# Optimization experiments

Hardware: AMD Instinct MI355X
Metric: run time of the kernel (lower is better)

Reference implementation:

```python
import jax, jax.numpy as jnp
import numpy as np
from jax import lax

B, N, C = 16, 16384, 90      # batch, anchors, classes
K = 100                      # per-class pre-NMS top-k
MAX_DET = 100                # final detections per image
IOU_THR = 0.5
SCORE_THR = 0.05


def setup_inputs() -> dict:
    key = jax.random.key(0)
    k1, k2, k3, k4 = jax.random.split(key, 4)
    box_encodings = jax.random.normal(k1, (B, N, 4), dtype=jnp.float32) * 0.5
    class_logits = jax.random.normal(k2, (B, N, C), dtype=jnp.float32) * 2.0 - 3.0
    # anchors as [ymin,xmin,ymax,xmax] in normalized coords
    centers = jax.random.uniform(k3, (N, 2), dtype=jnp.float32)             # (cy,cx)
    sizes = jax.random.uniform(k4, (N, 2), dtype=jnp.float32, minval=0.05, maxval=0.3)
    anchors = jnp.concatenate([centers - sizes / 2, centers + sizes / 2], axis=-1)
    return {"box_encodings": box_encodings, "class_logits": class_logits, "anchors": anchors}


def decode_boxes(enc, anchors):
    ymin, xmin, ymax, xmax = [anchors[:, i] for i in range(4)]
    ha, wa = ymax - ymin, xmax - xmin
    cya, cxa = (ymin + ymax) / 2, (xmin + xmax) / 2
    ty, tx, th, tw = enc[..., 0] / 10.0, enc[..., 1] / 10.0, enc[..., 2] / 5.0, enc[..., 3] / 5.0
    cy = ty * ha + cya
    cx = tx * wa + cxa
    h = jnp.exp(th) * ha
    w = jnp.exp(tw) * wa
    boxes = jnp.stack([cy - h / 2, cx - w / 2, cy + h / 2, cx + w / 2], axis=-1)
    return jnp.clip(boxes, 0.0, 1.0)  # [..., N, 4]


def pairwise_iou(b):  # b: [K,4]
    area = jnp.maximum(b[:, 2] - b[:, 0], 0) * jnp.maximum(b[:, 3] - b[:, 1], 0)
    iy = jnp.maximum(jnp.minimum(b[:, None, 2], b[None, :, 2]) - jnp.maximum(b[:, None, 0], b[None, :, 0]), 0)
    ix = jnp.maximum(jnp.minimum(b[:, None, 3], b[None, :, 3]) - jnp.maximum(b[:, None, 1], b[None, :, 1]), 0)
    inter = iy * ix
    union = area[:, None] + area[None, :] - inter
    return inter / jnp.maximum(union, 1e-8)


def nms_one_class(boxes, scores_c):  # boxes [N,4], scores_c [N]
    vals, idx = lax.top_k(scores_c, K)           # sorted descending
    bk = boxes[idx]                               # [K,4]
    iou = pairwise_iou(bk)                        # [K,K]
    def step(keep, i):
        supp = jnp.any(keep & (iou[i] >= IOU_THR))
        ki = (vals[i] > SCORE_THR) & (~supp)
        return keep.at[i].set(ki), None
    keep, _ = lax.scan(step, jnp.zeros((K,), bool), jnp.arange(K))
    return bk, vals * keep                        # suppressed -> score 0


def postprocess_one(boxes, scores):  # boxes [N,4], scores [N,C]
    bx_ck, sc_ck = jax.vmap(nms_one_class, in_axes=(None, 1))(boxes, scores)  # [C,K,4],[C,K]
    cls_ck = jnp.broadcast_to(jnp.arange(C, dtype=jnp.float32)[:, None], (C, K))
    sc_f = sc_ck.reshape(-1)
    fsc, fidx = lax.top_k(sc_f, MAX_DET)
    fbx = bx_ck.reshape(-1, 4)[fidx]
    fcl = cls_ck.reshape(-1)[fidx]
    return jnp.concatenate([fbx, fcl[:, None], fsc[:, None]], axis=-1)  # [MAX_DET, 6]


def reference(box_encodings, class_logits, anchors):
    boxes = decode_boxes(box_encodings, anchors)       # [B,N,4]
    scores = jax.nn.sigmoid(class_logits)              # [B,N,C]
    combined = jax.vmap(postprocess_one)(boxes, scores)  # [B,MAX_DET,6] = boxes|class|score
    return combined
```

## Files before the change

kernel.cpp:

```cpp
#include <hip/hip_runtime.h>
#include <stdint.h>
#include <math.h>

#define B_ 16
#define NN 16384
#define C_ 90
#define KSEL 100
#define MAXD 100
#define MFLAT (C_ * KSEL)
#define NPAIR 128
#define ZKEY 0x80000000u


__device__ __forceinline__ uint32_t fkey(float f) {
  uint32_t u = __float_as_uint(f);
  return (u & 0x80000000u) ? ~u : (u | 0x80000000u);
}
__device__ __forceinline__ float keyinv(uint32_t k) {
  uint32_t u = (k & 0x80000000u) ? (k & 0x7FFFFFFFu) : ~k;
  return __uint_as_float(u);
}

__device__ __forceinline__ uint32_t blockSum512(uint32_t v, uint32_t* red, uint32_t* s_total) {
  int tid = threadIdx.x;
#pragma unroll
  for (int o = 32; o > 0; o >>= 1) v += __shfl_down(v, o, 64);
  if ((tid & 63) == 0) red[tid >> 6] = v;
  __syncthreads();
  if (tid == 0) {
    uint32_t s = 0;
#pragma unroll
    for (int i = 0; i < 8; ++i) s += red[i];
    *s_total = s;
  }
  __syncthreads();
  return *s_total;
}

__global__ __launch_bounds__(256) void transpose_key16_kernel(const float* __restrict__ logits,
                                                              uint16_t* __restrict__ keys16T) {
  __shared__ uint32_t tile[128 * 91];
  int b = blockIdx.y;
  int n0 = blockIdx.x * 128;
  const float4* src4 = reinterpret_cast<const float4*>(logits + ((size_t)b * NN + n0) * C_);
  for (int p = threadIdx.x; p < 2880; p += 256) {
    float4 v = src4[p];
    int e = p * 4;
    float vv[4] = {v.x, v.y, v.z, v.w};
#pragma unroll
    for (int j = 0; j < 4; ++j) {
      int ee = e + j;
      tile[(ee / C_) * 91 + (ee % C_)] = fkey(vv[j]);
    }
  }
  __syncthreads();
  uint16_t* dstb = keys16T + (size_t)b * C_ * NN + n0;
  for (int q = threadIdx.x; q < C_ * 16; q += 256) {
    int c = q >> 4, g = q & 15;
    int nn2 = g * 8;
    uint4 o;
    o.x = (tile[(nn2 + 0) * 91 + c] >> 16) | (tile[(nn2 + 1) * 91 + c] & 0xFFFF0000u);
    o.y = (tile[(nn2 + 2) * 91 + c] >> 16) | (tile[(nn2 + 3) * 91 + c] & 0xFFFF0000u);
    o.z = (tile[(nn2 + 4) * 91 + c] >> 16) | (tile[(nn2 + 5) * 91 + c] & 0xFFFF0000u);
    o.w = (tile[(nn2 + 6) * 91 + c] >> 16) | (tile[(nn2 + 7) * 91 + c] & 0xFFFF0000u);
    reinterpret_cast<uint4*>(dstb + (size_t)c * NN)[g] = o;
  }
}

template <int TR>
__global__ __launch_bounds__(512, 8) void select_kernel(
    const uint16_t* __restrict__ keys16T,
    const float* __restrict__ logits,
    uint32_t* __restrict__ candPacked,
    uint32_t* __restrict__ candCount) {
  __shared__ uint32_t hist[2048];
  __shared__ uint32_t sc[512];
  __shared__ uint32_t ws8[64];
  __shared__ int s_bsel;
  __shared__ uint32_t s_Sincl, s_Sexcl;
  __shared__ uint32_t red[8];
  __shared__ uint32_t s_total;
  __shared__ uint32_t s_cnt;

  const int c = blockIdx.x, b = blockIdx.y;
  const int tid = threadIdx.x;

  uint32_t keyw[16];
  if (TR) {
    const uint4* src4 = reinterpret_cast<const uint4*>(keys16T + ((size_t)b * C_ + c) * NN);
#pragma unroll
    for (int q = 0; q < 4; ++q) {
      uint4 kv = src4[q * 512 + tid];
      keyw[4 * q + 0] = kv.x; keyw[4 * q + 1] = kv.y;
      keyw[4 * q + 2] = kv.z; keyw[4 * q + 3] = kv.w;
    }
  } else {
    const float* src = logits + (size_t)b * NN * C_ + c;
#pragma unroll
    for (int m = 0; m < 16; ++m) {
      uint32_t i0 = (uint32_t)((((m >> 2) * 512 + tid) * 8) + ((m & 3) * 2));
      uint32_t klo = fkey(src[(size_t)i0 * C_]) >> 16;
      uint32_t khi = fkey(src[(size_t)(i0 + 1) * C_]) >> 16;
      keyw[m] = klo | (khi << 16);
    }
  }

  reinterpret_cast<uint4*>(hist)[tid] = make_uint4(0u, 0u, 0u, 0u);
  __syncthreads();
#pragma unroll
  for (int m = 0; m < 16; ++m) {
    uint32_t w = keyw[m];
    atomicAdd(&hist[(w & 0xFFFFu) >> 5], 1u);
    atomicAdd(&hist[w >> 21], 1u);
  }
  __syncthreads();

  uint32_t m_above = 0;
  uint32_t need = 100u;
  uint32_t cut16 = 0;
  int found = 0;
  int tiepath = 0;
  uint32_t V16 = 0, Texact = NN - 1;

  {
    uint32_t h0 = hist[4 * tid], h1 = hist[4 * tid + 1];
    uint32_t h2 = hist[4 * tid + 2], h3 = hist[4 * tid + 3];
    sc[tid] = h0 + h1 + h2 + h3;
    if (tid == 0) s_bsel = -1;
    __syncthreads();
    if (tid < 64) {
      uint32_t w = 0;
      int base = tid * 8;
#pragma unroll
      for (int i = 0; i < 8; ++i) w += sc[base + i];
#pragma unroll
      for (int off = 1; off < 64; off <<= 1) {
        uint32_t v = __shfl_down(w, off, 64);
        if (tid + off < 64) w += v;
      }
      ws8[tid] = w;
    }
    __syncthreads();
    {
      int g = tid >> 3;
      uint32_t above = (g < 63) ? ws8[g + 1] : 0u;
      for (int j = (g << 3) + 7; j > tid; --j) above += sc[j];
      uint32_t run = above;
      int best = -1;
      uint32_t bi = 0, be = 0;
      uint32_t hh[4] = {h0, h1, h2, h3};
#pragma unroll
      for (int p = 3; p >= 0; --p) {
        uint32_t h = hh[p];
        run += h;
        if (best < 0 && run >= need) { best = 4 * tid + p; bi = run; be = run - h; }
      }
      if (best >= 0) atomicMax(&s_bsel, best);
      __syncthreads();
      if (best >= 0 && best == s_bsel) { s_Sincl = bi; s_Sexcl = be; }
    }
    __syncthreads();

    uint32_t bsel = (uint32_t)s_bsel;
    uint32_t Sincl = s_Sincl, Sexcl = s_Sexcl;
    if (Sincl <= (uint32_t)NPAIR) {
      cut16 = bsel << 5;
      found = 1;
    } else {
      m_above = Sexcl;
      need = 100u - m_above;
      __syncthreads();
      if (tid < 8) reinterpret_cast<uint4*>(hist)[tid] = make_uint4(0u, 0u, 0u, 0u);
      __syncthreads();
#pragma unroll
      for (int m = 0; m < 16; ++m) {
        uint32_t w = keyw[m];
        uint32_t klo = w & 0xFFFFu, khi = w >> 16;
        if ((klo >> 5) == bsel) atomicAdd(&hist[klo & 31u], 1u);
        if ((khi >> 5) == bsel) atomicAdd(&hist[khi & 31u], 1u);
      }
      __syncthreads();
      uint32_t run = 0;
      int b1 = -1;
      uint32_t Si = 0, Se = 0;
      for (int p = 31; p >= 0; --p) {
        uint32_t h = hist[p];
        run += h;
        if (b1 < 0 && run >= need) { b1 = p; Si = run; Se = run - h; }
      }
      uint32_t cutv = (bsel << 5) | (uint32_t)b1;
      if (m_above + Si <= (uint32_t)NPAIR) {
        cut16 = cutv;
        found = 1;
      } else {
        tiepath = 1;
        V16 = cutv;
        m_above += Se;
        uint32_t r = 100u - m_above;
        uint32_t lo2 = 0, hi2 = NN - 1;
        while (lo2 < hi2) {
          uint32_t mid2 = lo2 + ((hi2 - lo2) >> 1);
          uint32_t cnt = 0;
#pragma unroll
          for (int m = 0; m < 16; ++m) {
            uint32_t w = keyw[m];
            uint32_t i0 = (uint32_t)((((m >> 2) * 512 + tid) * 8) + ((m & 3) * 2));
            cnt += ((w & 0xFFFFu) == V16 && i0 <= mid2) ? 1u : 0u;
            cnt += ((w >> 16) == V16 && (i0 + 1) <= mid2) ? 1u : 0u;
          }
          uint32_t tot = blockSum512(cnt, red, &s_total);
          if (tot >= r) hi2 = mid2; else lo2 = mid2 + 1;
        }
        Texact = lo2;
      }
    }
  }

  if (tid == 0) s_cnt = 0;
  __syncthreads();
  uint32_t* outp = candPacked + (size_t)(b * C_ + c) * NPAIR;
#pragma unroll
  for (int m = 0; m < 16; ++m) {
    uint32_t w = keyw[m];
    uint32_t i0 = (uint32_t)((((m >> 2) * 512 + tid) * 8) + ((m & 3) * 2));
    uint32_t klo = w & 0xFFFFu, khi = w >> 16;
    bool t0 = tiepath ? (klo > V16 || (klo == V16 && i0 <= Texact)) : (klo >= cut16);
    bool t1 = tiepath ? (khi > V16 || (khi == V16 && (i0 + 1) <= Texact)) : (khi >= cut16);
    if (t0) {
      uint32_t p = atomicAdd(&s_cnt, 1u);
      if (p < (uint32_t)NPAIR) outp[p] = (klo << 16) | i0;
    }
    if (t1) {
      uint32_t p = atomicAdd(&s_cnt, 1u);
      if (p < (uint32_t)NPAIR) outp[p] = (khi << 16) | (i0 + 1);
    }
  }
  __syncthreads();
  if (tid == 0) candCount[b * C_ + c] = (s_cnt > (uint32_t)NPAIR) ? (uint32_t)NPAIR : s_cnt;
}

__global__ __launch_bounds__(256, 8) void sort_nms_kernel(
    const uint32_t* __restrict__ candPacked,
    const uint32_t* __restrict__ candCount,
    const float* __restrict__ logits,
    const float* __restrict__ enc,
    const float* __restrict__ anchors,
    float* __restrict__ candBox,
    float* __restrict__ candScore) {
  __shared__ unsigned long long ck[NPAIR];
  __shared__ float p_box[NPAIR][4];
  __shared__ float p_area[NPAIR];
  __shared__ unsigned long long M[NPAIR][2];
  __shared__ uint32_t s_sl[NPAIR];
  __shared__ unsigned long long s_keepw[2];

  const int c = blockIdx.x, b = blockIdx.y;
  const int tid = threadIdx.x;
  const int bc = b * C_ + c;
  const uint32_t cnt = candCount[bc];

  unsigned long long myKey = 0ull;
  bool myOk = false;
  float ry1 = 0, rx1 = 0, ry2 = 0, rx2 = 0, rar = 0;

  if (tid < NPAIR) {
    int s = tid;
    uint32_t v = candPacked[(size_t)bc * NPAIR + s];
    int n = (s < (int)cnt) ? (int)(v & 0x3FFFu) : 0;
    float x = logits[((size_t)b * NN + n) * C_ + c];
    float sv = 1.0f / (1.0f + expf(-x));
    myOk = (sv > 0.05f);
    myKey = (s < (int)cnt)
        ? (((unsigned long long)fkey(sv) << 32) |
           (unsigned long long)((((uint32_t)(NN - 1 - n)) << 7) | (uint32_t)s))
        : (unsigned long long)s;
    ck[s] = myKey;
  } else {
    int s = tid - NPAIR;
    uint32_t v = candPacked[(size_t)bc * NPAIR + s];
    int n = (s < (int)cnt) ? (int)(v & 0x3FFFu) : 0;
    float4 e = reinterpret_cast<const float4*>(enc)[(size_t)b * NN + n];
    float4 a = reinterpret_cast<const float4*>(anchors)[n];
    float ha = a.z - a.x, wa = a.w - a.y;
    float cya = (a.x + a.z) * 0.5f, cxa = (a.y + a.w) * 0.5f;
    float cy = (e.x / 10.0f) * ha + cya;
    float cx = (e.y / 10.0f) * wa + cxa;
    float h = expf(e.z / 5.0f) * ha;
    float w = expf(e.w / 5.0f) * wa;
    ry1 = fminf(fmaxf(cy - h * 0.5f, 0.0f), 1.0f);
    rx1 = fminf(fmaxf(cx - w * 0.5f, 0.0f), 1.0f);
    ry2 = fminf(fmaxf(cy + h * 0.5f, 0.0f), 1.0f);
    rx2 = fminf(fmaxf(cx + w * 0.5f, 0.0f), 1.0f);
    rar = fmaxf(ry2 - ry1, 0.0f) * fmaxf(rx2 - rx1, 0.0f);
    float4* pb = reinterpret_cast<float4*>(p_box[s]);
    *pb = make_float4(ry1, rx1, ry2, rx2);
    p_area[s] = rar;
  }
  __syncthreads();

  if (tid < NPAIR) {
    uint32_t rank = 0;
#pragma unroll 8
    for (int j = 0; j < NPAIR; ++j) rank += (ck[j] > myKey) ? 1u : 0u;
    s_sl[rank] = (uint32_t)tid | (myOk ? 256u : 0u);
  } else {
    int s = tid - NPAIR;
    unsigned long long m0 = 0ull, m1 = 0ull;
#pragma unroll 4
    for (int q = 0; q < NPAIR; ++q) {
      float4 bq = *reinterpret_cast<const float4*>(p_box[q]);
      float aq = p_area[q];
      float ta = fmaxf(fminf(bq.z, ry2) - fmaxf(bq.x, ry1), 0.0f) *
                 fmaxf(fminf(bq.w, rx2) - fmaxf(bq.y, rx1), 0.0f);
      float un = fmaxf(aq + rar - ta, 1e-8f);
      bool hit = (ta / un >= 0.5f);
      if (q < 64) m0 |= (unsigned long long)hit << q;
      else        m1 |= (unsigned long long)hit << (q - 64);
    }
    M[s][0] = m0; M[s][1] = m1;
  }
  __syncthreads();

  if (tid < 64) {
    unsigned long long supp0 = 0, supp1 = 0, k0 = 0, k1 = 0;
#pragma unroll 4
    for (int j = 0; j < KSEL; ++j) {
      uint32_t e = s_sl[j];
      int sl = (int)(e & 127u);
      unsigned long long r0 = M[sl][0], r1 = M[sl][1];
      bool suppd = (sl < 64) ? ((supp0 >> sl) & 1ull) : ((supp1 >> (sl - 64)) & 1ull);
      bool pass = (e & 256u) && !suppd;
      if (pass) {
        supp0 |= r0; supp1 |= r1;
        if (j < 64) k0 |= 1ull << j; else k1 |= 1ull << (j - 64);
      }
    }
    if (tid == 0) { s_keepw[0] = k0; s_keepw[1] = k1; }
  }
  __syncthreads();

  if (tid < KSEL) {
    int slot = (int)(s_sl[tid] & 127u);
    unsigned long long keyv = ck[slot];
    bool kept = (tid < 64) ? ((s_keepw[0] >> tid) & 1ull)
                           : ((s_keepw[1] >> (tid - 64)) & 1ull);
    size_t base = (size_t)bc * KSEL + tid;
    candScore[base] = kept ? keyinv((uint32_t)(keyv >> 32)) : 0.0f;
    float* cb = candBox + base * 4;
    cb[0] = p_box[slot][0]; cb[1] = p_box[slot][1];
    cb[2] = p_box[slot][2]; cb[3] = p_box[slot][3];
  }
}

#define FT_NT 512
#define FT_SLOTS 18
#define FT_NW 8
__global__ __launch_bounds__(FT_NT) void final_topk_kernel(
    const float* __restrict__ candScore,
    const float* __restrict__ candBox,
    float* __restrict__ out) {
  __shared__ uint32_t skey[FT_NT * FT_SLOTS];
  __shared__ uint32_t hist[FT_NW * 2048];
  __shared__ uint32_t sc[512];
  __shared__ uint32_t ws8[64];
  __shared__ int s_bsel;
  __shared__ uint32_t s_Sincl, s_Sexcl;
  __shared__ uint32_t red[8];
  __shared__ uint32_t s_total;
  __shared__ uint32_t s_cnt;
  __shared__ unsigned long long ck[128];

  int b = blockIdx.x, tid = threadIdx.x;
  const int wid = tid >> 6;
  const float* src = candScore + (size_t)b * MFLAT;

  uint32_t nzc = 0;
  for (int q = 0; q < FT_SLOTS; ++q) {
    int idx = q * FT_NT + tid;
    uint32_t k = (idx < MFLAT) ? fkey(src[idx]) : 0u;
    skey[idx] = k;
    nzc += (k > ZKEY) ? 1u : 0u;
  }
  __syncthreads();
  uint32_t nz = blockSum512(nzc, red, &s_total);

  uint32_t cutHi = 0, m_above = 0, cut32 = 0;
  int found = 0, tiepath = 0;
  uint32_t V32 = 0, Texact = (uint32_t)(MFLAT - 1);
  uint32_t tie_r = 0;

  if (nz < 100u) {
    tiepath = 1;
    V32 = ZKEY;
    tie_r = 100u - nz;
  } else {
    for (int lvl = 0; lvl < 3; ++lvl) {
      const int shiftLo = (lvl == 0) ? 21 : (lvl == 1) ? 10 : 0;
      const uint32_t mask = (lvl == 2) ? 0x3FFu : 0x7FFu;
      const int nbits = (lvl == 2) ? 10 : 11;

      for (int i = tid; i < FT_NW * 512; i += FT_NT)
        reinterpret_cast<uint4*>(hist)[i] = make_uint4(0u, 0u, 0u, 0u);
      __syncthreads();
      uint32_t* myh = hist + wid * 2048;
      for (int q = 0; q < FT_SLOTS; ++q) {
        uint32_t k = skey[q * FT_NT + tid];
        bool in = (k > ZKEY) && ((lvl == 0) ? true : ((k >> (shiftLo + nbits)) == cutHi));
        if (in) atomicAdd(&myh[(k >> shiftLo) & mask], 1u);
      }
      __syncthreads();

      const uint32_t need = 100u - m_above;

      uint32_t h0 = 0, h1 = 0, h2 = 0, h3 = 0;
#pragma unroll
      for (int w = 0; w < FT_NW; ++w) {
        uint4 a = *reinterpret_cast<const uint4*>(hist + w * 2048 + 4 * tid);
        h0 += a.x; h1 += a.y; h2 += a.z; h3 += a.w;
      }
      sc[tid] = h0 + h1 + h2 + h3;
      if (tid == 0) s_bsel = -1;
      __syncthreads();
      if (tid < 64) {
        uint32_t w = 0;
        int base = tid * 8;
#pragma unroll
        for (int i = 0; i < 8; ++i) w += sc[base + i];
#pragma unroll
        for (int off = 1; off < 64; off <<= 1) {
          uint32_t v = __shfl_down(w, off, 64);
          if (tid + off < 64) w += v;
        }
        ws8[tid] = w;
      }
      __syncthreads();
      {
        int g = tid >> 3;
        uint32_t above = (g < 63) ? ws8[g + 1] : 0u;
        for (int j = (g << 3) + 7; j > tid; --j) above += sc[j];
        uint32_t run = above;
        int best = -1;
        uint32_t bi = 0, be = 0;
        uint32_t hh[4] = {h0, h1, h2, h3};
#pragma unroll
        for (int p = 3; p >= 0; --p) {
          uint32_t h = hh[p];
          run += h;
          if (best < 0 && run >= need) { best = 4 * tid + p; bi = run; be = run - h; }
        }
        if (best >= 0) atomicMax(&s_bsel, best);
        __syncthreads();
        if (best >= 0 && best == s_bsel) { s_Sincl = bi; s_Sexcl = be; }
      }
      __syncthreads();

      uint32_t bsel = (uint32_t)s_bsel;
      cutHi = (cutHi << nbits) | bsel;
      if (m_above + s_Sincl <= 128u) {
        cut32 = cutHi << shiftLo;
        found = 1;
        break;
      }
      m_above += s_Sexcl;
      __syncthreads();
    }

    if (!found) {
      tiepath = 1;
      V32 = cutHi;
      tie_r = 100u - m_above;
    }
  }

  if (tiepath) {
    uint32_t lo2 = 0, hi2 = (uint32_t)(MFLAT - 1);
    while (lo2 < hi2) {
      uint32_t mid2 = lo2 + ((hi2 - lo2) >> 1);
      uint32_t cnt = 0;
      for (int q = 0; q < FT_SLOTS; ++q) {
        uint32_t idx = (uint32_t)(q * FT_NT + tid);
        cnt += (skey[idx] == V32 && idx <= mid2) ? 1u : 0u;
      }
      uint32_t tot = blockSum512(cnt, red, &s_total);
      if (tot >= tie_r) hi2 = mid2; else lo2 = mid2 + 1;
    }
    Texact = lo2;
  }

  if (tid == 0) s_cnt = 0;
  __syncthreads();
  for (int q = 0; q < FT_SLOTS; ++q) {
    uint32_t idx = (uint32_t)(q * FT_NT + tid);
    uint32_t k = skey[idx];
    bool take = tiepath ? (k > V32 || (k == V32 && idx <= Texact))
                        : (k > ZKEY && k >= cut32);
    if (take) {
      uint32_t p = atomicAdd(&s_cnt, 1u);
      if (p < 128u)
        ck[p] = ((unsigned long long)k << 32) | (unsigned long long)(~idx);
    }
  }
  __syncthreads();
  if (tid < 128 && (uint32_t)tid >= s_cnt) ck[tid] = 0ull;
  __syncthreads();

  for (int kk = 2; kk <= 128; kk <<= 1) {
    for (int j = kk >> 1; j > 0; j >>= 1) {
      if (tid < 128) {
        int ixj = tid ^ j;
        if (ixj > tid) {
          unsigned long long a = ck[tid], bb = ck[ixj];
          if ((a < bb) == ((tid & kk) == 0)) { ck[tid] = bb; ck[ixj] = a; }
        }
      }
      __syncthreads();
    }
  }

  if (tid < MAXD) {
    unsigned long long keyv = ck[tid];
    int f = (int)(~(uint32_t)(keyv & 0xFFFFFFFFull));
    int c = f / KSEL;
    float sc2 = keyinv((uint32_t)(keyv >> 32));
    const float* cb = candBox + ((size_t)b * MFLAT + f) * 4;
    float* o = out + ((size_t)b * MAXD + tid) * 6;
    o[0] = cb[0]; o[1] = cb[1]; o[2] = cb[2]; o[3] = cb[3];
    o[4] = (float)c; o[5] = sc2;
  }
}

extern "C" void kernel_launch(void* const* d_in, const int* in_sizes, int n_in,
                              void* d_out, int out_size, void* d_ws, size_t ws_size,
                              hipStream_t stream) {
  const float* enc = (const float*)d_in[0];
  const float* logits = (const float*)d_in[1];
  const float* anchors = (const float*)d_in[2];
  float* out = (float*)d_out;
  char* ws = (char*)d_ws;

  size_t off = 0;
  float* candBox = (float*)(ws + off);   off += (size_t)B_ * C_ * KSEL * 4 * sizeof(float);
  float* candScore = (float*)(ws + off); off += (size_t)B_ * C_ * KSEL * sizeof(float);
  uint32_t* candPacked = (uint32_t*)(ws + off);
  off += (size_t)B_ * C_ * NPAIR * sizeof(uint32_t);
  uint32_t* candCount = (uint32_t*)(ws + off); off += (size_t)B_ * C_ * sizeof(uint32_t);
  off = (off + 255) & ~(size_t)255;
  uint16_t* keys16T = (uint16_t*)(ws + off);
  size_t needT = off + (size_t)B_ * C_ * NN * sizeof(uint16_t);
  int transposed = (ws_size >= needT) ? 1 : 0;

  if (transposed) {
    transpose_key16_kernel<<<dim3(NN / 128, B_), 256, 0, stream>>>(logits, keys16T);
    select_kernel<1><<<dim3(C_, B_), 512, 0, stream>>>(keys16T, logits, candPacked, candCount);
  } else {
    select_kernel<0><<<dim3(C_, B_), 512, 0, stream>>>(keys16T, logits, candPacked, candCount);
  }

  sort_nms_kernel<<<dim3(C_, B_), 256, 0, stream>>>(candPacked, candCount, logits,
                                                    enc, anchors, candBox, candScore);

  final_topk_kernel<<<B_, FT_NT, 0, stream>>>(candScore, candBox, out);
}
```

Measured before the change: 134.7 us.

## Fuse per-class candidate selection with sort and NMS in one kernel

Merges the select kernel and the sort/NMS kernel into a single 512-thread block per (batch, class). Candidates now stay in shared memory instead of going through a global candPacked/candCount round trip, and one kernel launch is removed. In exchange the fused block uses more shared memory, which may reduce occupancy. Half of its threads sit idle during the NMS phase, and the 8-blocks launch bound may now be harder to meet.

After: 146.9 us. +9.1%, slower.

```diff
diff --git a/kernel.cpp b/kernel.cpp
--- a/kernel.cpp
+++ b/kernel.cpp
@@ -68,11 +68,13 @@
 }
 
 template <int TR>
-__global__ __launch_bounds__(512, 8) void select_kernel(
+__global__ __launch_bounds__(512, 8) void select_nms_kernel(
     const uint16_t* __restrict__ keys16T,
     const float* __restrict__ logits,
-    uint32_t* __restrict__ candPacked,
-    uint32_t* __restrict__ candCount) {
+    const float* __restrict__ enc,
+    const float* __restrict__ anchors,
+    float* __restrict__ candBox,
+    float* __restrict__ candScore) {
   __shared__ uint32_t hist[2048];
   __shared__ uint32_t sc[512];
   __shared__ uint32_t ws8[64];
@@ -81,9 +83,17 @@
   __shared__ uint32_t red[8];
   __shared__ uint32_t s_total;
   __shared__ uint32_t s_cnt;
+  __shared__ uint32_t s_cand[NPAIR];
+  __shared__ unsigned long long ck[NPAIR];
+  __shared__ float p_box[NPAIR][4];
+  __shared__ float p_area[NPAIR];
+  __shared__ uint32_t s_sl[NPAIR];
+  __shared__ unsigned long long M[NPAIR][2];
+  __shared__ unsigned long long s_keepw[2];
 
   const int c = blockIdx.x, b = blockIdx.y;
   const int tid = threadIdx.x;
+  const int bc = b * C_ + c;
 
   uint32_t keyw[16];
   if (TR) {
@@ -200,15 +210,15 @@
         uint32_t lo2 = 0, hi2 = NN - 1;
         while (lo2 < hi2) {
           uint32_t mid2 = lo2 + ((hi2 - lo2) >> 1);
-          uint32_t cnt = 0;
+          uint32_t cnt2 = 0;
 #pragma unroll
           for (int m = 0; m < 16; ++m) {
             uint32_t w = keyw[m];
             uint32_t i0 = (uint32_t)((((m >> 2) * 512 + tid) * 8) + ((m & 3) * 2));
-            cnt += ((w & 0xFFFFu) == V16 && i0 <= mid2) ? 1u : 0u;
-            cnt += ((w >> 16) == V16 && (i0 + 1) <= mid2) ? 1u : 0u;
+            cnt2 += ((w & 0xFFFFu) == V16 && i0 <= mid2) ? 1u : 0u;
+            cnt2 += ((w >> 16) == V16 && (i0 + 1) <= mid2) ? 1u : 0u;
           }
-          uint32_t tot = blockSum512(cnt, red, &s_total);
+          uint32_t tot = blockSum512(cnt2, red, &s_total);
           if (tot >= r) hi2 = mid2; else lo2 = mid2 + 1;
         }
         Texact = lo2;
@@ -218,7 +228,6 @@
 
   if (tid == 0) s_cnt = 0;
   __syncthreads();
-  uint32_t* outp = candPacked + (size_t)(b * C_ + c) * NPAIR;
 #pragma unroll
   for (int m = 0; m < 16; ++m) {
     uint32_t w = keyw[m];
@@ -228,36 +237,16 @@
     bool t1 = tiepath ? (khi > V16 || (khi == V16 && (i0 + 1) <= Texact)) : (khi >= cut16);
     if (t0) {
       uint32_t p = atomicAdd(&s_cnt, 1u);
-      if (p < (uint32_t)NPAIR) outp[p] = (klo << 16) | i0;
+      if (p < (uint32_t)NPAIR) s_cand[p] = (klo << 16) | i0;
     }
     if (t1) {
       uint32_t p = atomicAdd(&s_cnt, 1u);
-      if (p < (uint32_t)NPAIR) outp[p] = (khi << 16) | (i0 + 1);
-    }
-  }
-  __syncthreads();
-  if (tid == 0) candCount[b * C_ + c] = (s_cnt > (uint32_t)NPAIR) ? (uint32_t)NPAIR : s_cnt;
-}
-
-__global__ __launch_bounds__(256, 8) void sort_nms_kernel(
-    const uint32_t* __restrict__ candPacked,
-    const uint32_t* __restrict__ candCount,
-    const float* __restrict__ logits,
-    const float* __restrict__ enc,
-    const float* __restrict__ anchors,
-    float* __restrict__ candBox,
-    float* __restrict__ candScore) {
-  __shared__ unsigned long long ck[NPAIR];
-  __shared__ float p_box[NPAIR][4];
-  __shared__ float p_area[NPAIR];
-  __shared__ unsigned long long M[NPAIR][2];
-  __shared__ uint32_t s_sl[NPAIR];
-  __shared__ unsigned long long s_keepw[2];
-
-  const int c = blockIdx.x, b = blockIdx.y;
-  const int tid = threadIdx.x;
-  const int bc = b * C_ + c;
-  const uint32_t cnt = candCount[bc];
+      if (p < (uint32_t)NPAIR) s_cand[p] = (khi << 16) | (i0 + 1);
+    }
+  }
+  __syncthreads();
+  const uint32_t cnt = (s_cnt > (uint32_t)NPAIR) ? (uint32_t)NPAIR : s_cnt;
+
 
   unsigned long long myKey = 0ull;
   bool myOk = false;
@@ -265,7 +254,7 @@
 
   if (tid < NPAIR) {
     int s = tid;
-    uint32_t v = candPacked[(size_t)bc * NPAIR + s];
+    uint32_t v = (s < (int)cnt) ? s_cand[s] : 0u;
     int n = (s < (int)cnt) ? (int)(v & 0x3FFFu) : 0;
     float x = logits[((size_t)b * NN + n) * C_ + c];
     float sv = 1.0f / (1.0f + expf(-x));
@@ -275,9 +264,9 @@
            (unsigned long long)((((uint32_t)(NN - 1 - n)) << 7) | (uint32_t)s))
         : (unsigned long long)s;
     ck[s] = myKey;
-  } else {
+  } else if (tid < 2 * NPAIR) {
     int s = tid - NPAIR;
-    uint32_t v = candPacked[(size_t)bc * NPAIR + s];
+    uint32_t v = (s < (int)cnt) ? s_cand[s] : 0u;
     int n = (s < (int)cnt) ? (int)(v & 0x3FFFu) : 0;
     float4 e = reinterpret_cast<const float4*>(enc)[(size_t)b * NN + n];
     float4 a = reinterpret_cast<const float4*>(anchors)[n];
@@ -303,7 +292,7 @@
 #pragma unroll 8
     for (int j = 0; j < NPAIR; ++j) rank += (ck[j] > myKey) ? 1u : 0u;
     s_sl[rank] = (uint32_t)tid | (myOk ? 256u : 0u);
-  } else {
+  } else if (tid < 2 * NPAIR) {
     int s = tid - NPAIR;
     unsigned long long m0 = 0ull, m1 = 0ull;
 #pragma unroll 4
@@ -541,9 +530,6 @@
   size_t off = 0;
   float* candBox = (float*)(ws + off);   off += (size_t)B_ * C_ * KSEL * 4 * sizeof(float);
   float* candScore = (float*)(ws + off); off += (size_t)B_ * C_ * KSEL * sizeof(float);
-  uint32_t* candPacked = (uint32_t*)(ws + off);
-  off += (size_t)B_ * C_ * NPAIR * sizeof(uint32_t);
-  uint32_t* candCount = (uint32_t*)(ws + off); off += (size_t)B_ * C_ * sizeof(uint32_t);
   off = (off + 255) & ~(size_t)255;
   uint16_t* keys16T = (uint16_t*)(ws + off);
   size_t needT = off + (size_t)B_ * C_ * NN * sizeof(uint16_t);
@@ -551,13 +537,12 @@
 
   if (transposed) {
     transpose_key16_kernel<<<dim3(NN / 128, B_), 256, 0, stream>>>(logits, keys16T);
-    select_kernel<1><<<dim3(C_, B_), 512, 0, stream>>>(keys16T, logits, candPacked, candCount);
+    select_nms_kernel<1><<<dim3(C_, B_), 512, 0, stream>>>(keys16T, logits, enc, anchors,
+                                                           candBox, candScore);
   } else {
-    select_kernel<0><<<dim3(C_, B_), 512, 0, stream>>>(keys16T, logits, candPacked, candCount);
-  }
-
-  sort_nms_kernel<<<dim3(C_, B_), 256, 0, stream>>>(candPacked, candCount, logits,
-                                                    enc, anchors, candBox, candScore);
+    select_nms_kernel<0><<<dim3(C_, B_), 512, 0, stream>>>(keys16T, logits, enc, anchors,
+                                                           candBox, candScore);
+  }
 
   final_topk_kernel<<<B_, FT_NT, 0, stream>>>(candScore, candBox, out);
 }
```
